# Kernel optimization log

Measured on AMD Instinct MI355X. Metric: run time of the kernel, lower is better.

## Reference

```python
import jax, jax.numpy as jnp
import numpy as np

N = 100000   # nodes
E = 1600000  # edges (avg degree 16)
D = 128      # in_feats
H = 128      # n_hidden
C = 64       # n_classes


def setup_inputs() -> dict:
    key = jax.random.key(0)
    ks = jax.random.split(key, 9)
    x = jax.random.normal(ks[0], (N, D), dtype=jnp.float32)
    src = jax.random.randint(ks[1], (E,), 0, N, dtype=jnp.int32)
    dst = jax.random.randint(ks[2], (E,), 0, N, dtype=jnp.int32)
    s = 1.0 / np.sqrt(D)
    W1 = jax.random.uniform(ks[3], (H, D), jnp.float32, -s, s)
    b1 = jax.random.uniform(ks[4], (H,), jnp.float32, -s, s)
    sh = 1.0 / np.sqrt(H)
    W2 = jax.random.uniform(ks[5], (H, H), jnp.float32, -sh, sh)
    b2 = jax.random.uniform(ks[6], (H,), jnp.float32, -sh, sh)
    W3 = jax.random.uniform(ks[7], (C, H), jnp.float32, -sh, sh)
    b3 = jax.random.uniform(ks[8], (C,), jnp.float32, -sh, sh)
    return {"x": x, "src": src, "dst": dst,
            "W1": W1, "b1": b1, "W2": W2, "b2": b2, "W3": W3, "b3": b3}


def reference(x, src, dst, W1, b1, W2, b2, W3, b3):
    n = x.shape[0]
    # in-degrees of destination nodes (DGL g.in_degrees())
    deg = jax.ops.segment_sum(jnp.ones_like(dst, dtype=x.dtype), dst, num_segments=n)
    norm = 1.0 / (deg + 1.0)  # [N]

    def sage_gcn(h, W, b, act):
        # gather src features, sum into dst (copy_u + sum reduce)
        m = jax.ops.segment_sum(h[src], dst, num_segments=n)  # [N, d]
        h_neigh = (m + h) * norm[:, None]                      # include self, /(deg+1)
        o = h_neigh @ W.T + b                                  # fc_neigh
        return jax.nn.relu(o) if act else o

    h = sage_gcn(x, W1, b1, True)
    h = sage_gcn(h, W2, b2, True)   # dropout is identity in eval mode
    return sage_gcn(h, W3, b3, False)
```

## Files before the change

kernel.cpp:

```cpp
#include <hip/hip_runtime.h>
#include <hip/hip_fp16.h>

typedef _Float16 f16x8 __attribute__((ext_vector_type(8)));
typedef _Float16 f16x4 __attribute__((ext_vector_type(4)));
typedef float    f32x4 __attribute__((ext_vector_type(4)));


#define PSHIFT 6
#define PNODES 64
#define BMAX   2048
#define NBLK   64

__global__ __launch_bounds__(512) void k_hist(const int* __restrict__ dst, int E, int chunk,
                                              int B, int* __restrict__ histT) {
    __shared__ int hist[BMAX];
    int blk = blockIdx.x, t = threadIdx.x;
    for (int k = t; k < B; k += 512) hist[k] = 0;
    __syncthreads();
    int lo = blk * chunk, hi = min(lo + chunk, E);
    for (int i = lo + t; i < hi; i += 512) atomicAdd(&hist[dst[i] >> PSHIFT], 1);
    __syncthreads();
    for (int k = t; k < B; k += 512) histT[k * NBLK + blk] = hist[k];
}

__global__ __launch_bounds__(256) void k_scanA(const int* __restrict__ histT, int total,
                                               int* __restrict__ psum) {
    __shared__ int sd[256];
    int t = threadIdx.x;
    int base = blockIdx.x * 1024 + t * 4;
    int s = 0;
    if (base + 3 < total) {
        int4 v = *(const int4*)(histT + base);
        s = v.x + v.y + v.z + v.w;
    } else {
        for (int j = 0; j < 4; j++) if (base + j < total) s += histT[base + j];
    }
    sd[t] = s;
    __syncthreads();
    for (int off = 128; off > 0; off >>= 1) {
        if (t < off) sd[t] += sd[t + off];
        __syncthreads();
    }
    if (t == 0) psum[blockIdx.x] = sd[0];
}

__global__ __launch_bounds__(128) void k_scanB(const int* __restrict__ psum, int G,
                                               int* __restrict__ pbase,
                                               int* __restrict__ bbase, int B,
                                               int* __restrict__ offsets, int n, int E) {
    __shared__ int sd[128];
    int t = threadIdx.x;
    int v = (t < G) ? psum[t] : 0;
    sd[t] = v;
    __syncthreads();
    int acc = v;
    for (int off = 1; off < 128; off <<= 1) {
        int u = (t >= off) ? sd[t - off] : 0;
        __syncthreads();
        acc += u;
        sd[t] = acc;
        __syncthreads();
    }
    if (t < G) pbase[t] = acc - v;
    if (t == 0) { bbase[B] = E; offsets[n] = E; }
}

__global__ __launch_bounds__(256) void k_scanC(int* __restrict__ histT, int total,
                                               const int* __restrict__ pbase,
                                               int* __restrict__ bbase) {
    __shared__ int sd[256];
    int t = threadIdx.x;
    int base = blockIdx.x * 1024 + t * 4;
    int v[4];
    int s = 0;
    bool full = (base + 3 < total);
    if (full) {
        int4 q = *(const int4*)(histT + base);
        v[0] = q.x; v[1] = q.y; v[2] = q.z; v[3] = q.w;
        s = q.x + q.y + q.z + q.w;
    } else {
#pragma unroll
        for (int j = 0; j < 4; j++) { v[j] = (base + j < total) ? histT[base + j] : 0; s += v[j]; }
    }
    sd[t] = s;
    __syncthreads();
    int acc = s;
    for (int off = 1; off < 256; off <<= 1) {
        int u = (t >= off) ? sd[t - off] : 0;
        __syncthreads();
        acc += u;
        sd[t] = acc;
        __syncthreads();
    }
    int run = pbase[blockIdx.x] + (acc - s);
    int o[4];
#pragma unroll
    for (int j = 0; j < 4; j++) { o[j] = run; run += v[j]; }
    if (full) *(int4*)(histT + base) = make_int4(o[0], o[1], o[2], o[3]);
    else { for (int j = 0; j < 4; j++) if (base + j < total) histT[base + j] = o[j]; }
    if ((base & 63) == 0 && base < total) bbase[base >> 6] = o[0];
}

__global__ __launch_bounds__(512) void k_place(const int* __restrict__ src,
                                               const int* __restrict__ dst,
                                               const int* __restrict__ histT,
                                               int E, int chunk, int B,
                                               unsigned int* __restrict__ ebuf) {
    __shared__ int cur[BMAX];
    int blk = blockIdx.x, t = threadIdx.x;
    for (int k = t; k < B; k += 512) cur[k] = histT[k * NBLK + blk];
    __syncthreads();
    int lo = blk * chunk, hi = min(lo + chunk, E);
    for (int i = lo + t; i < hi; i += 512) {
        int d = dst[i], s = src[i];
        int k = d >> PSHIFT;
        int pos = atomicAdd(&cur[k], 1);
        ebuf[pos] = ((unsigned)(d & (PNODES - 1)) << 17) | (unsigned)s;
    }
}

__global__ __launch_bounds__(256) void k_binB(const unsigned int* __restrict__ ebuf,
                                              const int* __restrict__ bbase,
                                              int* __restrict__ offsets,
                                              float* __restrict__ norm,
                                              int* __restrict__ cols, int n) {
    __shared__ int hist[PNODES];
    __shared__ int lofs[PNODES];
    __shared__ int cur[PNODES];
    int b = blockIdx.x;
    int t = threadIdx.x;
    int base = bbase[b];
    int cnt = bbase[b + 1] - base;
    const unsigned int* bd = ebuf + base;

    if (t < PNODES) hist[t] = 0;
    __syncthreads();
    for (int e = t; e < cnt; e += 256) atomicAdd(&hist[bd[e] >> 17], 1);
    __syncthreads();
    if (t < PNODES) lofs[t] = hist[t];
    __syncthreads();
    for (int off = 1; off < PNODES; off <<= 1) {
        int v = 0;
        if (t < PNODES && t >= off) v = lofs[t - off];
        __syncthreads();
        if (t < PNODES) lofs[t] += v;
        __syncthreads();
    }
    if (t < PNODES) {
        int excl = lofs[t] - hist[t];
        cur[t] = excl;
        int node = (b << PSHIFT) + t;
        if (node < n) {
            offsets[node] = base + excl;
            norm[node] = 1.0f / ((float)hist[t] + 1.0f);
        }
    }
    __syncthreads();
    for (int e = t; e < cnt; e += 256) {
        unsigned v = bd[e];
        int local = v >> 17;
        int s = (int)(v & 0x1FFFF);
        int r = atomicAdd(&cur[local], 1);
        cols[base + r] = s;
    }
}


__global__ __launch_bounds__(256) void k_cvt(const float* __restrict__ x,
                                             _Float16* __restrict__ y, int total8) {
    int i = blockIdx.x * 256 + threadIdx.x;
    if (i >= total8) return;
    float4 a = ((const float4*)x)[i * 2];
    float4 b = ((const float4*)x)[i * 2 + 1];
    f16x8 o;
    o[0] = (_Float16)a.x; o[1] = (_Float16)a.y; o[2] = (_Float16)a.z; o[3] = (_Float16)a.w;
    o[4] = (_Float16)b.x; o[5] = (_Float16)b.y; o[6] = (_Float16)b.z; o[7] = (_Float16)b.w;
    ((f16x8*)y)[i] = o;
}


template <int KOUT, bool IN_F32>
__global__ __launch_bounds__(256) void k_gemm_mfma(const void* __restrict__ Ain,
                                                   const _Float16* __restrict__ Wh,
                                                   _Float16* __restrict__ outh, int n) {
    constexpr int NT = KOUT / 16;
    __shared__ _Float16 A_lds[128 * 136];
    __shared__ _Float16 W_lds[KOUT * 136];

    int tid  = threadIdx.x;
    int lane = tid & 63;
    int wave = tid >> 6;
    int m0   = blockIdx.x * 128;

    for (int i = tid; i < KOUT * 16; i += 256) {
        int r = i >> 4, c = i & 15;
        *(f16x8*)&W_lds[r * 136 + c * 8] = ((const f16x8*)(Wh + r * 128))[c];
    }
    if constexpr (IN_F32) {
        const float* A = (const float*)Ain;
        for (int i = tid; i < 2048; i += 256) {
            int r = i >> 4, c = i & 15;
            int gm = m0 + r;
            f16x8 v = {};
            if (gm < n) {
                float4 u0 = *(const float4*)(A + (size_t)gm * 128 + c * 8);
                float4 u1 = *(const float4*)(A + (size_t)gm * 128 + c * 8 + 4);
                v[0] = (_Float16)u0.x; v[1] = (_Float16)u0.y;
                v[2] = (_Float16)u0.z; v[3] = (_Float16)u0.w;
                v[4] = (_Float16)u1.x; v[5] = (_Float16)u1.y;
                v[6] = (_Float16)u1.z; v[7] = (_Float16)u1.w;
            }
            *(f16x8*)&A_lds[r * 136 + c * 8] = v;
        }
    } else {
        const _Float16* A = (const _Float16*)Ain;
        for (int i = tid; i < 2048; i += 256) {
            int r = i >> 4, c = i & 15;
            int gm = m0 + r;
            f16x8 v = {};
            if (gm < n) v = ((const f16x8*)(A + (size_t)gm * 128))[c];
            *(f16x8*)&A_lds[r * 136 + c * 8] = v;
        }
    }
    __syncthreads();

    int m0w = wave * 32;
    int lr  = lane & 15;
    int lk  = (lane >> 4) * 4;

    f32x4 acc[2][NT];
#pragma unroll
    for (int mi = 0; mi < 2; mi++)
#pragma unroll
        for (int ni = 0; ni < NT; ni++) acc[mi][ni] = (f32x4){0.f, 0.f, 0.f, 0.f};

#pragma unroll
    for (int kk = 0; kk < 8; kk++) {
        int k0 = kk * 16;
        f16x4 a0 = *(const f16x4*)&A_lds[(m0w + lr) * 136 + k0 + lk];
        f16x4 a1 = *(const f16x4*)&A_lds[(m0w + 16 + lr) * 136 + k0 + lk];
#pragma unroll
        for (int ni = 0; ni < NT; ni++) {
            f16x4 b = *(const f16x4*)&W_lds[(ni * 16 + lr) * 136 + k0 + lk];
            acc[0][ni] = __builtin_amdgcn_mfma_f32_16x16x16f16(a0, b, acc[0][ni], 0, 0, 0);
            acc[1][ni] = __builtin_amdgcn_mfma_f32_16x16x16f16(a1, b, acc[1][ni], 0, 0, 0);
        }
    }

    int orow = (lane >> 4) * 4;
#pragma unroll
    for (int mi = 0; mi < 2; mi++) {
#pragma unroll
        for (int r = 0; r < 4; r++) {
            int gm = m0 + m0w + mi * 16 + orow + r;
            if (gm < n) {
                _Float16* op = outh + (size_t)gm * KOUT + lr;
#pragma unroll
                for (int ni = 0; ni < NT; ni++)
                    op[ni * 16] = (_Float16)acc[mi][ni][r];
            }
        }
    }
}


__global__ __launch_bounds__(256) void k_agg128_br(const _Float16* __restrict__ g,
                                                   const int* __restrict__ offs,
                                                   const int* __restrict__ cols,
                                                   const float* __restrict__ norm,
                                                   const float* __restrict__ bias,
                                                   _Float16* __restrict__ hout, int n) {
    int node = blockIdx.x * 16 + (threadIdx.x >> 4);
    if (node >= n) return;
    int lane = threadIdx.x & 15;

    f16x8 sv = ((const f16x8*)(g + (size_t)node * 128))[lane];
    float acc[8];
#pragma unroll
    for (int j = 0; j < 8; j++) acc[j] = (float)sv[j];

    int p = offs[node], e = offs[node + 1];
    for (; p + 4 <= e; p += 4) {
        int c0 = cols[p], c1 = cols[p + 1], c2 = cols[p + 2], c3 = cols[p + 3];
        f16x8 a0 = ((const f16x8*)(g + (size_t)c0 * 128))[lane];
        f16x8 a1 = ((const f16x8*)(g + (size_t)c1 * 128))[lane];
        f16x8 a2 = ((const f16x8*)(g + (size_t)c2 * 128))[lane];
        f16x8 a3 = ((const f16x8*)(g + (size_t)c3 * 128))[lane];
#pragma unroll
        for (int j = 0; j < 8; j++)
            acc[j] += ((float)a0[j] + (float)a1[j]) + ((float)a2[j] + (float)a3[j]);
    }
    for (; p < e; p++) {
        f16x8 a = ((const f16x8*)(g + (size_t)cols[p] * 128))[lane];
#pragma unroll
        for (int j = 0; j < 8; j++) acc[j] += (float)a[j];
    }
    float nm = norm[node];
    float4 bb0 = ((const float4*)bias)[lane * 2];
    float4 bb1 = ((const float4*)bias)[lane * 2 + 1];
    float o[8];
    o[0] = acc[0] * nm + bb0.x; o[1] = acc[1] * nm + bb0.y;
    o[2] = acc[2] * nm + bb0.z; o[3] = acc[3] * nm + bb0.w;
    o[4] = acc[4] * nm + bb1.x; o[5] = acc[5] * nm + bb1.y;
    o[6] = acc[6] * nm + bb1.z; o[7] = acc[7] * nm + bb1.w;
    f16x8 ov;
#pragma unroll
    for (int j = 0; j < 8; j++) ov[j] = (_Float16)fmaxf(o[j], 0.f);
    ((f16x8*)(hout + (size_t)node * 128))[lane] = ov;
}

__global__ __launch_bounds__(256) void k_agg64_b(const _Float16* __restrict__ g,
                                                 const int* __restrict__ offs,
                                                 const int* __restrict__ cols,
                                                 const float* __restrict__ norm,
                                                 const float* __restrict__ bias,
                                                 float* __restrict__ out, int n) {
    int node = blockIdx.x * 32 + (threadIdx.x >> 3);
    if (node >= n) return;
    int lane = threadIdx.x & 7;

    f16x8 sv = ((const f16x8*)(g + (size_t)node * 64))[lane];
    float acc[8];
#pragma unroll
    for (int j = 0; j < 8; j++) acc[j] = (float)sv[j];

    int p = offs[node], e = offs[node + 1];
    for (; p + 4 <= e; p += 4) {
        int c0 = cols[p], c1 = cols[p + 1], c2 = cols[p + 2], c3 = cols[p + 3];
        f16x8 a0 = ((const f16x8*)(g + (size_t)c0 * 64))[lane];
        f16x8 a1 = ((const f16x8*)(g + (size_t)c1 * 64))[lane];
        f16x8 a2 = ((const f16x8*)(g + (size_t)c2 * 64))[lane];
        f16x8 a3 = ((const f16x8*)(g + (size_t)c3 * 64))[lane];
#pragma unroll
        for (int j = 0; j < 8; j++)
            acc[j] += ((float)a0[j] + (float)a1[j]) + ((float)a2[j] + (float)a3[j]);
    }
    for (; p < e; p++) {
        f16x8 a = ((const f16x8*)(g + (size_t)cols[p] * 64))[lane];
#pragma unroll
        for (int j = 0; j < 8; j++) acc[j] += (float)a[j];
    }
    float nm = norm[node];
    float4 bb0 = ((const float4*)bias)[lane * 2];
    float4 bb1 = ((const float4*)bias)[lane * 2 + 1];
    float* op = out + (size_t)node * 64 + lane * 8;
    *(float4*)op = make_float4(acc[0] * nm + bb0.x, acc[1] * nm + bb0.y,
                               acc[2] * nm + bb0.z, acc[3] * nm + bb0.w);
    *(float4*)(op + 4) = make_float4(acc[4] * nm + bb1.x, acc[5] * nm + bb1.y,
                                     acc[6] * nm + bb1.z, acc[7] * nm + bb1.w);
}


extern "C" void kernel_launch(void* const* d_in, const int* in_sizes, int n_in,
                              void* d_out, int out_size, void* d_ws, size_t ws_size,
                              hipStream_t stream) {
    const float* x  = (const float*)d_in[0];
    const int*  src = (const int*)d_in[1];
    const int*  dst = (const int*)d_in[2];
    const float* W1 = (const float*)d_in[3];
    const float* b1 = (const float*)d_in[4];
    const float* W2 = (const float*)d_in[5];
    const float* b2 = (const float*)d_in[6];
    const float* W3 = (const float*)d_in[7];
    const float* b3 = (const float*)d_in[8];
    float* out = (float*)d_out;

    int n = in_sizes[0] / 128;
    int E = in_sizes[1];
    int B = (n + PNODES - 1) >> PSHIFT;
    int total = B * NBLK;
    int chunk = (E + NBLK - 1) / NBLK;
    int G1 = (total + 1023) / 1024;

    char* ws = (char*)d_ws;
    size_t off = 0;
    auto alloc = [&](size_t bytes) -> char* {
        char* p = ws + off;
        off += (bytes + 255) & ~(size_t)255;
        return p;
    };
    int*      bbase   = (int*)alloc(((size_t)B + 1) * 4);
    int*      offsets = (int*)alloc(((size_t)n + 1) * 4);
    float*    norm    = (float*)alloc((size_t)n * 4);
    int*      psum    = (int*)alloc(256 * 4);
    int*      pbase   = (int*)alloc(256 * 4);
    int*      cols    = (int*)alloc((size_t)E * 4);
    _Float16* w1h     = (_Float16*)alloc(128 * 128 * 2);
    _Float16* w2h     = (_Float16*)alloc(128 * 128 * 2);
    _Float16* w3h     = (_Float16*)alloc(64 * 128 * 2);
    _Float16* bufA    = (_Float16*)alloc((size_t)n * 128 * 2);
    _Float16* bufB    = (_Float16*)alloc((size_t)n * 128 * 2);

    unsigned int* ebuf  = (unsigned int*)bufA;
    int*          histT = (int*)((char*)bufA + (size_t)8 * 1024 * 1024);

    k_cvt<<<8, 256, 0, stream>>>(W1, w1h, 2048);
    k_cvt<<<8, 256, 0, stream>>>(W2, w2h, 2048);
    k_cvt<<<4, 256, 0, stream>>>(W3, w3h, 1024);

    k_hist <<<NBLK, 512, 0, stream>>>(dst, E, chunk, B, histT);
    k_scanA<<<G1, 256, 0, stream>>>(histT, total, psum);
    k_scanB<<<1, 128, 0, stream>>>(psum, G1, pbase, bbase, B, offsets, n, E);
    k_scanC<<<G1, 256, 0, stream>>>(histT, total, pbase, bbase);
    k_place<<<NBLK, 512, 0, stream>>>(src, dst, histT, E, chunk, B, ebuf);
    k_binB <<<B, 256, 0, stream>>>(ebuf, bbase, offsets, norm, cols, n);

    int nblkG  = (n + 127) / 128;
    int nblkA  = (n + 15) / 16;
    int nblkA6 = (n + 31) / 32;

    k_gemm_mfma<128, true><<<nblkG, 256, 0, stream>>>(x, w1h, bufA, n);
    k_agg128_br<<<nblkA, 256, 0, stream>>>(bufA, offsets, cols, norm, b1, bufB, n);
    k_gemm_mfma<128, false><<<nblkG, 256, 0, stream>>>(bufB, w2h, bufA, n);
    k_agg128_br<<<nblkA, 256, 0, stream>>>(bufA, offsets, cols, norm, b2, bufB, n);
    k_gemm_mfma<64, false><<<nblkG, 256, 0, stream>>>(bufB, w3h, bufA, n);
    k_agg64_b<<<nblkA6, 256, 0, stream>>>(bufA, offsets, cols, norm, b3, out, n);
}
```

Before: 283.0 us.

## Fuse weight conversion into GEMM, unroll gathers by 8, remap 64-wide aggregation

Removes the three separate weight-conversion kernels by converting fp32 weights to fp16 while loading them into LDS inside each GEMM block. This saves three launches but repeats the conversion in every block. Both aggregation kernels gain an 8-way unrolled neighbour loop so more independent gathers are in flight per thread. The 64-wide aggregation now uses 16 lanes per node with 4-element loads instead of 8 lanes with 8-element loads, giving more threads per node and fewer nodes per block.

```diff
diff --git a/kernel.cpp b/kernel.cpp
--- a/kernel.cpp
+++ b/kernel.cpp
@@ -166,22 +166,9 @@
 }
 
 
-__global__ __launch_bounds__(256) void k_cvt(const float* __restrict__ x,
-                                             _Float16* __restrict__ y, int total8) {
-    int i = blockIdx.x * 256 + threadIdx.x;
-    if (i >= total8) return;
-    float4 a = ((const float4*)x)[i * 2];
-    float4 b = ((const float4*)x)[i * 2 + 1];
-    f16x8 o;
-    o[0] = (_Float16)a.x; o[1] = (_Float16)a.y; o[2] = (_Float16)a.z; o[3] = (_Float16)a.w;
-    o[4] = (_Float16)b.x; o[5] = (_Float16)b.y; o[6] = (_Float16)b.z; o[7] = (_Float16)b.w;
-    ((f16x8*)y)[i] = o;
-}
-
-
 template <int KOUT, bool IN_F32>
 __global__ __launch_bounds__(256) void k_gemm_mfma(const void* __restrict__ Ain,
-                                                   const _Float16* __restrict__ Wh,
+                                                   const float* __restrict__ W,
                                                    _Float16* __restrict__ outh, int n) {
     constexpr int NT = KOUT / 16;
     __shared__ _Float16 A_lds[128 * 136];
@@ -194,7 +181,14 @@
 
     for (int i = tid; i < KOUT * 16; i += 256) {
         int r = i >> 4, c = i & 15;
-        *(f16x8*)&W_lds[r * 136 + c * 8] = ((const f16x8*)(Wh + r * 128))[c];
+        float4 u0 = *(const float4*)(W + (size_t)r * 128 + c * 8);
+        float4 u1 = *(const float4*)(W + (size_t)r * 128 + c * 8 + 4);
+        f16x8 v;
+        v[0] = (_Float16)u0.x; v[1] = (_Float16)u0.y;
+        v[2] = (_Float16)u0.z; v[3] = (_Float16)u0.w;
+        v[4] = (_Float16)u1.x; v[5] = (_Float16)u1.y;
+        v[6] = (_Float16)u1.z; v[7] = (_Float16)u1.w;
+        *(f16x8*)&W_lds[r * 136 + c * 8] = v;
     }
     if constexpr (IN_F32) {
         const float* A = (const float*)Ain;
@@ -280,6 +274,22 @@
     for (int j = 0; j < 8; j++) acc[j] = (float)sv[j];
 
     int p = offs[node], e = offs[node + 1];
+    for (; p + 8 <= e; p += 8) {
+        int c0 = cols[p],     c1 = cols[p + 1], c2 = cols[p + 2], c3 = cols[p + 3];
+        int c4 = cols[p + 4], c5 = cols[p + 5], c6 = cols[p + 6], c7 = cols[p + 7];
+        f16x8 a0 = ((const f16x8*)(g + (size_t)c0 * 128))[lane];
+        f16x8 a1 = ((const f16x8*)(g + (size_t)c1 * 128))[lane];
+        f16x8 a2 = ((const f16x8*)(g + (size_t)c2 * 128))[lane];
+        f16x8 a3 = ((const f16x8*)(g + (size_t)c3 * 128))[lane];
+        f16x8 a4 = ((const f16x8*)(g + (size_t)c4 * 128))[lane];
+        f16x8 a5 = ((const f16x8*)(g + (size_t)c5 * 128))[lane];
+        f16x8 a6 = ((const f16x8*)(g + (size_t)c6 * 128))[lane];
+        f16x8 a7 = ((const f16x8*)(g + (size_t)c7 * 128))[lane];
+#pragma unroll
+        for (int j = 0; j < 8; j++)
+            acc[j] += (((float)a0[j] + (float)a1[j]) + ((float)a2[j] + (float)a3[j]))
+                    + (((float)a4[j] + (float)a5[j]) + ((float)a6[j] + (float)a7[j]));
+    }
     for (; p + 4 <= e; p += 4) {
         int c0 = cols[p], c1 = cols[p + 1], c2 = cols[p + 2], c3 = cols[p + 3];
         f16x8 a0 = ((const f16x8*)(g + (size_t)c0 * 128))[lane];
@@ -315,39 +325,52 @@
                                                  const float* __restrict__ norm,
                                                  const float* __restrict__ bias,
                                                  float* __restrict__ out, int n) {
-    int node = blockIdx.x * 32 + (threadIdx.x >> 3);
+    int node = blockIdx.x * 16 + (threadIdx.x >> 4);
     if (node >= n) return;
-    int lane = threadIdx.x & 7;
-
-    f16x8 sv = ((const f16x8*)(g + (size_t)node * 64))[lane];
-    float acc[8];
-#pragma unroll
-    for (int j = 0; j < 8; j++) acc[j] = (float)sv[j];
+    int lane = threadIdx.x & 15;
+
+    f16x4 sv = ((const f16x4*)(g + (size_t)node * 64))[lane];
+    float acc[4];
+#pragma unroll
+    for (int j = 0; j < 4; j++) acc[j] = (float)sv[j];
 
     int p = offs[node], e = offs[node + 1];
+    for (; p + 8 <= e; p += 8) {
+        int c0 = cols[p],     c1 = cols[p + 1], c2 = cols[p + 2], c3 = cols[p + 3];
+        int c4 = cols[p + 4], c5 = cols[p + 5], c6 = cols[p + 6], c7 = cols[p + 7];
+        f16x4 a0 = ((const f16x4*)(g + (size_t)c0 * 64))[lane];
+        f16x4 a1 = ((const f16x4*)(g + (size_t)c1 * 64))[lane];
+        f16x4 a2 = ((const f16x4*)(g + (size_t)c2 * 64))[lane];
+        f16x4 a3 = ((const f16x4*)(g + (size_t)c3 * 64))[lane];
+        f16x4 a4 = ((const f16x4*)(g + (size_t)c4 * 64))[lane];
+        f16x4 a5 = ((const f16x4*)(g + (size_t)c5 * 64))[lane];
+        f16x4 a6 = ((const f16x4*)(g + (size_t)c6 * 64))[lane];
+        f16x4 a7 = ((const f16x4*)(g + (size_t)c7 * 64))[lane];
+#pragma unroll
+        for (int j = 0; j < 4; j++)
+            acc[j] += (((float)a0[j] + (float)a1[j]) + ((float)a2[j] + (float)a3[j]))
+                    + (((float)a4[j] + (float)a5[j]) + ((float)a6[j] + (float)a7[j]));
+    }
     for (; p + 4 <= e; p += 4) {
         int c0 = cols[p], c1 = cols[p + 1], c2 = cols[p + 2], c3 = cols[p + 3];
-        f16x8 a0 = ((const f16x8*)(g + (size_t)c0 * 64))[lane];
-        f16x8 a1 = ((const f16x8*)(g + (size_t)c1 * 64))[lane];
-        f16x8 a2 = ((const f16x8*)(g + (size_t)c2 * 64))[lane];
-        f16x8 a3 = ((const f16x8*)(g + (size_t)c3 * 64))[lane];
-#pragma unroll
-        for (int j = 0; j < 8; j++)
+        f16x4 a0 = ((const f16x4*)(g + (size_t)c0 * 64))[lane];
+        f16x4 a1 = ((const f16x4*)(g + (size_t)c1 * 64))[lane];
+        f16x4 a2 = ((const f16x4*)(g + (size_t)c2 * 64))[lane];
+        f16x4 a3 = ((const f16x4*)(g + (size_t)c3 * 64))[lane];
+#pragma unroll
+        for (int j = 0; j < 4; j++)
             acc[j] += ((float)a0[j] + (float)a1[j]) + ((float)a2[j] + (float)a3[j]);
     }
     for (; p < e; p++) {
-        f16x8 a = ((const f16x8*)(g + (size_t)cols[p] * 64))[lane];
-#pragma unroll
-        for (int j = 0; j < 8; j++) acc[j] += (float)a[j];
+        f16x4 a = ((const f16x4*)(g + (size_t)cols[p] * 64))[lane];
+#pragma unroll
+        for (int j = 0; j < 4; j++) acc[j] += (float)a[j];
     }
     float nm = norm[node];
-    float4 bb0 = ((const float4*)bias)[lane * 2];
-    float4 bb1 = ((const float4*)bias)[lane * 2 + 1];
-    float* op = out + (size_t)node * 64 + lane * 8;
-    *(float4*)op = make_float4(acc[0] * nm + bb0.x, acc[1] * nm + bb0.y,
-                               acc[2] * nm + bb0.z, acc[3] * nm + bb0.w);
-    *(float4*)(op + 4) = make_float4(acc[4] * nm + bb1.x, acc[5] * nm + bb1.y,
-                                     acc[6] * nm + bb1.z, acc[7] * nm + bb1.w);
+    float4 bb = ((const float4*)bias)[lane];
+    float* op = out + (size_t)node * 64 + lane * 4;
+    *(float4*)op = make_float4(acc[0] * nm + bb.x, acc[1] * nm + bb.y,
+                               acc[2] * nm + bb.z, acc[3] * nm + bb.w);
 }
 
 
@@ -385,18 +408,11 @@
     int*      psum    = (int*)alloc(256 * 4);
     int*      pbase   = (int*)alloc(256 * 4);
     int*      cols    = (int*)alloc((size_t)E * 4);
-    _Float16* w1h     = (_Float16*)alloc(128 * 128 * 2);
-    _Float16* w2h     = (_Float16*)alloc(128 * 128 * 2);
-    _Float16* w3h     = (_Float16*)alloc(64 * 128 * 2);
     _Float16* bufA    = (_Float16*)alloc((size_t)n * 128 * 2);
     _Float16* bufB    = (_Float16*)alloc((size_t)n * 128 * 2);
 
     unsigned int* ebuf  = (unsigned int*)bufA;
     int*          histT = (int*)((char*)bufA + (size_t)8 * 1024 * 1024);
-
-    k_cvt<<<8, 256, 0, stream>>>(W1, w1h, 2048);
-    k_cvt<<<8, 256, 0, stream>>>(W2, w2h, 2048);
-    k_cvt<<<4, 256, 0, stream>>>(W3, w3h, 1024);
 
     k_hist <<<NBLK, 512, 0, stream>>>(dst, E, chunk, B, histT);
     k_scanA<<<G1, 256, 0, stream>>>(histT, total, psum);
@@ -405,14 +421,13 @@
     k_place<<<NBLK, 512, 0, stream>>>(src, dst, histT, E, chunk, B, ebuf);
     k_binB <<<B, 256, 0, stream>>>(ebuf, bbase, offsets, norm, cols, n);
 
-    int nblkG  = (n + 127) / 128;
-    int nblkA  = (n + 15) / 16;
-    int nblkA6 = (n + 31) / 32;
-
-    k_gemm_mfma<128, true><<<nblkG, 256, 0, stream>>>(x, w1h, bufA, n);
+    int nblkG = (n + 127) / 128;
+    int nblkA = (n + 15) / 16;
+
+    k_gemm_mfma<128, true><<<nblkG, 256, 0, stream>>>(x, W1, bufA, n);
     k_agg128_br<<<nblkA, 256, 0, stream>>>(bufA, offsets, cols, norm, b1, bufB, n);
-    k_gemm_mfma<128, false><<<nblkG, 256, 0, stream>>>(bufB, w2h, bufA, n);
+    k_gemm_mfma<128, false><<<nblkG, 256, 0, stream>>>(bufB, W2, bufA, n);
     k_agg128_br<<<nblkA, 256, 0, stream>>>(bufA, offsets, cols, norm, b2, bufB, n);
-    k_gemm_mfma<64, false><<<nblkG, 256, 0, stream>>>(bufB, w3h, bufA, n);
-    k_agg64_b<<<nblkA6, 256, 0, stream>>>(bufA, offsets, cols, norm, b3, out, n);
-}
+    k_gemm_mfma<64, false><<<nblkG, 256, 0, stream>>>(bufB, W3, bufA, n);
+    k_agg64_b<<<nblkA, 256, 0, stream>>>(bufA, offsets, cols, norm, b3, out, n);
+}
```

New measurement: 280.3 us. Within noise of the previous version (-1.0%).

## Slice aggregation by feature columns, split GEMM output, merge weight conversions, widen histogram

Applied to the files above, without the earlier changes.

The aggregation kernels now assign each block a 16-column feature slice for 128 nodes. Each node is handled by two threads reading 16 bytes each, where previously 16 or 8 threads shared one node's full row. Column indices are read with nontemporal loads. The idea is to keep each slice's gather working set small enough to stay in cache, at the cost of re-reading the CSR indices once per slice. The GEMM now processes output columns in 64-wide halves to reduce weight LDS. The three weight conversions are merged into one launch, and the histogram/placement grid doubles to 128 blocks, with the scan adjusted to match.

```diff
diff --git a/kernel.cpp b/kernel.cpp
--- a/kernel.cpp
+++ b/kernel.cpp
@@ -9,7 +9,7 @@
 #define PSHIFT 6
 #define PNODES 64
 #define BMAX   2048
-#define NBLK   64
+#define NBLK   128
 
 __global__ __launch_bounds__(512) void k_hist(const int* __restrict__ dst, int E, int chunk,
                                               int B, int* __restrict__ histT) {
@@ -44,17 +44,17 @@
     if (t == 0) psum[blockIdx.x] = sd[0];
 }
 
-__global__ __launch_bounds__(128) void k_scanB(const int* __restrict__ psum, int G,
+__global__ __launch_bounds__(256) void k_scanB(const int* __restrict__ psum, int G,
                                                int* __restrict__ pbase,
                                                int* __restrict__ bbase, int B,
                                                int* __restrict__ offsets, int n, int E) {
-    __shared__ int sd[128];
+    __shared__ int sd[256];
     int t = threadIdx.x;
     int v = (t < G) ? psum[t] : 0;
     sd[t] = v;
     __syncthreads();
     int acc = v;
-    for (int off = 1; off < 128; off <<= 1) {
+    for (int off = 1; off < 256; off <<= 1) {
         int u = (t >= off) ? sd[t - off] : 0;
         __syncthreads();
         acc += u;
@@ -98,7 +98,7 @@
     for (int j = 0; j < 4; j++) { o[j] = run; run += v[j]; }
     if (full) *(int4*)(histT + base) = make_int4(o[0], o[1], o[2], o[3]);
     else { for (int j = 0; j < 4; j++) if (base + j < total) histT[base + j] = o[j]; }
-    if ((base & 63) == 0 && base < total) bbase[base >> 6] = o[0];
+    if ((base & (NBLK - 1)) == 0 && base < total) bbase[base / NBLK] = o[0];
 }
 
 __global__ __launch_bounds__(512) void k_place(const int* __restrict__ src,
@@ -166,35 +166,41 @@
 }
 
 
-__global__ __launch_bounds__(256) void k_cvt(const float* __restrict__ x,
-                                             _Float16* __restrict__ y, int total8) {
+__global__ __launch_bounds__(256) void k_cvtW(const float* __restrict__ W1,
+                                              const float* __restrict__ W2,
+                                              const float* __restrict__ W3,
+                                              _Float16* __restrict__ w16) {
     int i = blockIdx.x * 256 + threadIdx.x;
-    if (i >= total8) return;
-    float4 a = ((const float4*)x)[i * 2];
-    float4 b = ((const float4*)x)[i * 2 + 1];
-    f16x8 o;
-    o[0] = (_Float16)a.x; o[1] = (_Float16)a.y; o[2] = (_Float16)a.z; o[3] = (_Float16)a.w;
-    o[4] = (_Float16)b.x; o[5] = (_Float16)b.y; o[6] = (_Float16)b.z; o[7] = (_Float16)b.w;
-    ((f16x8*)y)[i] = o;
+    if (i >= 5120) return;
+    int idx = i * 8;
+    const float* src;
+    if (idx < 16384)      src = W1 + idx;
+    else if (idx < 32768) src = W2 + (idx - 16384);
+    else                  src = W3 + (idx - 32768);
+    float4 a = *(const float4*)src;
+    float4 b = *(const float4*)(src + 4);
+    f16x8 v;
+    v[0] = (_Float16)a.x; v[1] = (_Float16)a.y; v[2] = (_Float16)a.z; v[3] = (_Float16)a.w;
+    v[4] = (_Float16)b.x; v[5] = (_Float16)b.y; v[6] = (_Float16)b.z; v[7] = (_Float16)b.w;
+    *(f16x8*)(w16 + idx) = v;
 }
 
 
 template <int KOUT, bool IN_F32>
 __global__ __launch_bounds__(256) void k_gemm_mfma(const void* __restrict__ Ain,
-                                                   const _Float16* __restrict__ Wh,
+                                                   const _Float16* __restrict__ W16,
                                                    _Float16* __restrict__ outh, int n) {
-    constexpr int NT = KOUT / 16;
     __shared__ _Float16 A_lds[128 * 136];
-    __shared__ _Float16 W_lds[KOUT * 136];
+    __shared__ _Float16 W_lds[64 * 136];
 
     int tid  = threadIdx.x;
     int lane = tid & 63;
     int wave = tid >> 6;
     int m0   = blockIdx.x * 128;
 
-    for (int i = tid; i < KOUT * 16; i += 256) {
+    for (int i = tid; i < 64 * 16; i += 256) {
         int r = i >> 4, c = i & 15;
-        *(f16x8*)&W_lds[r * 136 + c * 8] = ((const f16x8*)(Wh + r * 128))[c];
+        *(f16x8*)&W_lds[r * 136 + c * 8] = *(const f16x8*)(W16 + (size_t)r * 128 + c * 8);
     }
     if constexpr (IN_F32) {
         const float* A = (const float*)Ain;
@@ -227,77 +233,97 @@
     int m0w = wave * 32;
     int lr  = lane & 15;
     int lk  = (lane >> 4) * 4;
-
-    f32x4 acc[2][NT];
-#pragma unroll
-    for (int mi = 0; mi < 2; mi++)
-#pragma unroll
-        for (int ni = 0; ni < NT; ni++) acc[mi][ni] = (f32x4){0.f, 0.f, 0.f, 0.f};
-
-#pragma unroll
-    for (int kk = 0; kk < 8; kk++) {
-        int k0 = kk * 16;
-        f16x4 a0 = *(const f16x4*)&A_lds[(m0w + lr) * 136 + k0 + lk];
-        f16x4 a1 = *(const f16x4*)&A_lds[(m0w + 16 + lr) * 136 + k0 + lk];
-#pragma unroll
-        for (int ni = 0; ni < NT; ni++) {
-            f16x4 b = *(const f16x4*)&W_lds[(ni * 16 + lr) * 136 + k0 + lk];
-            acc[0][ni] = __builtin_amdgcn_mfma_f32_16x16x16f16(a0, b, acc[0][ni], 0, 0, 0);
-            acc[1][ni] = __builtin_amdgcn_mfma_f32_16x16x16f16(a1, b, acc[1][ni], 0, 0, 0);
-        }
-    }
-
     int orow = (lane >> 4) * 4;
-#pragma unroll
-    for (int mi = 0; mi < 2; mi++) {
-#pragma unroll
-        for (int r = 0; r < 4; r++) {
-            int gm = m0 + m0w + mi * 16 + orow + r;
-            if (gm < n) {
-                _Float16* op = outh + (size_t)gm * KOUT + lr;
-#pragma unroll
-                for (int ni = 0; ni < NT; ni++)
-                    op[ni * 16] = (_Float16)acc[mi][ni][r];
+
+#pragma unroll
+    for (int hf = 0; hf < KOUT / 64; hf++) {
+        if (hf > 0) {
+            __syncthreads();
+            for (int i = tid; i < 64 * 16; i += 256) {
+                int r = i >> 4, c = i & 15;
+                *(f16x8*)&W_lds[r * 136 + c * 8] =
+                    *(const f16x8*)(W16 + (size_t)(hf * 64 + r) * 128 + c * 8);
             }
-        }
-    }
-}
-
-
-__global__ __launch_bounds__(256) void k_agg128_br(const _Float16* __restrict__ g,
-                                                   const int* __restrict__ offs,
-                                                   const int* __restrict__ cols,
-                                                   const float* __restrict__ norm,
-                                                   const float* __restrict__ bias,
-                                                   _Float16* __restrict__ hout, int n) {
-    int node = blockIdx.x * 16 + (threadIdx.x >> 4);
+            __syncthreads();
+        }
+
+        f32x4 acc[2][4];
+#pragma unroll
+        for (int mi = 0; mi < 2; mi++)
+#pragma unroll
+            for (int ni = 0; ni < 4; ni++) acc[mi][ni] = (f32x4){0.f, 0.f, 0.f, 0.f};
+
+#pragma unroll
+        for (int kk = 0; kk < 8; kk++) {
+            int k0 = kk * 16;
+            f16x4 a0 = *(const f16x4*)&A_lds[(m0w + lr) * 136 + k0 + lk];
+            f16x4 a1 = *(const f16x4*)&A_lds[(m0w + 16 + lr) * 136 + k0 + lk];
+#pragma unroll
+            for (int ni = 0; ni < 4; ni++) {
+                f16x4 b = *(const f16x4*)&W_lds[(ni * 16 + lr) * 136 + k0 + lk];
+                acc[0][ni] = __builtin_amdgcn_mfma_f32_16x16x16f16(a0, b, acc[0][ni], 0, 0, 0);
+                acc[1][ni] = __builtin_amdgcn_mfma_f32_16x16x16f16(a1, b, acc[1][ni], 0, 0, 0);
+            }
+        }
+
+#pragma unroll
+        for (int mi = 0; mi < 2; mi++) {
+#pragma unroll
+            for (int r = 0; r < 4; r++) {
+                int gm = m0 + m0w + mi * 16 + orow + r;
+                if (gm < n) {
+                    _Float16* op = outh + (size_t)gm * KOUT + hf * 64 + lr;
+#pragma unroll
+                    for (int ni = 0; ni < 4; ni++)
+                        op[ni * 16] = (_Float16)acc[mi][ni][r];
+                }
+            }
+        }
+    }
+}
+
+
+__global__ __launch_bounds__(256) void k_agg128_slice(const _Float16* __restrict__ g,
+                                                      const int* __restrict__ offs,
+                                                      const int* __restrict__ cols,
+                                                      const float* __restrict__ norm,
+                                                      const float* __restrict__ bias,
+                                                      _Float16* __restrict__ hout, int n) {
+    int s     = blockIdx.x & 7;
+    int chunk = blockIdx.x >> 3;
+    int node  = chunk * 128 + (threadIdx.x >> 1);
     if (node >= n) return;
-    int lane = threadIdx.x & 15;
-
-    f16x8 sv = ((const f16x8*)(g + (size_t)node * 128))[lane];
+    int l2 = threadIdx.x & 1;
+    const _Float16* gs = g + s * 16 + l2 * 8;
+
+    f16x8 sv = *(const f16x8*)(gs + (size_t)node * 128);
     float acc[8];
 #pragma unroll
     for (int j = 0; j < 8; j++) acc[j] = (float)sv[j];
 
     int p = offs[node], e = offs[node + 1];
     for (; p + 4 <= e; p += 4) {
-        int c0 = cols[p], c1 = cols[p + 1], c2 = cols[p + 2], c3 = cols[p + 3];
-        f16x8 a0 = ((const f16x8*)(g + (size_t)c0 * 128))[lane];
-        f16x8 a1 = ((const f16x8*)(g + (size_t)c1 * 128))[lane];
-        f16x8 a2 = ((const f16x8*)(g + (size_t)c2 * 128))[lane];
-        f16x8 a3 = ((const f16x8*)(g + (size_t)c3 * 128))[lane];
+        int c0 = __builtin_nontemporal_load(cols + p);
+        int c1 = __builtin_nontemporal_load(cols + p + 1);
+        int c2 = __builtin_nontemporal_load(cols + p + 2);
+        int c3 = __builtin_nontemporal_load(cols + p + 3);
+        f16x8 a0 = *(const f16x8*)(gs + (size_t)c0 * 128);
+        f16x8 a1 = *(const f16x8*)(gs + (size_t)c1 * 128);
+        f16x8 a2 = *(const f16x8*)(gs + (size_t)c2 * 128);
+        f16x8 a3 = *(const f16x8*)(gs + (size_t)c3 * 128);
 #pragma unroll
         for (int j = 0; j < 8; j++)
             acc[j] += ((float)a0[j] + (float)a1[j]) + ((float)a2[j] + (float)a3[j]);
     }
     for (; p < e; p++) {
-        f16x8 a = ((const f16x8*)(g + (size_t)cols[p] * 128))[lane];
+        int c = __builtin_nontemporal_load(cols + p);
+        f16x8 a = *(const f16x8*)(gs + (size_t)c * 128);
 #pragma unroll
         for (int j = 0; j < 8; j++) acc[j] += (float)a[j];
     }
     float nm = norm[node];
-    float4 bb0 = ((const float4*)bias)[lane * 2];
-    float4 bb1 = ((const float4*)bias)[lane * 2 + 1];
+    float4 bb0 = *(const float4*)(bias + s * 16 + l2 * 8);
+    float4 bb1 = *(const float4*)(bias + s * 16 + l2 * 8 + 4);
     float o[8];
     o[0] = acc[0] * nm + bb0.x; o[1] = acc[1] * nm + bb0.y;
     o[2] = acc[2] * nm + bb0.z; o[3] = acc[3] * nm + bb0.w;
@@ -306,44 +332,51 @@
     f16x8 ov;
 #pragma unroll
     for (int j = 0; j < 8; j++) ov[j] = (_Float16)fmaxf(o[j], 0.f);
-    ((f16x8*)(hout + (size_t)node * 128))[lane] = ov;
-}
-
-__global__ __launch_bounds__(256) void k_agg64_b(const _Float16* __restrict__ g,
-                                                 const int* __restrict__ offs,
-                                                 const int* __restrict__ cols,
-                                                 const float* __restrict__ norm,
-                                                 const float* __restrict__ bias,
-                                                 float* __restrict__ out, int n) {
-    int node = blockIdx.x * 32 + (threadIdx.x >> 3);
+    *(f16x8*)(hout + (size_t)node * 128 + s * 16 + l2 * 8) = ov;
+}
+
+__global__ __launch_bounds__(256) void k_agg64_slice(const _Float16* __restrict__ g,
+                                                     const int* __restrict__ offs,
+                                                     const int* __restrict__ cols,
+                                                     const float* __restrict__ norm,
+                                                     const float* __restrict__ bias,
+                                                     float* __restrict__ out, int n) {
+    int s     = blockIdx.x & 3;
+    int chunk = blockIdx.x >> 2;
+    int node  = chunk * 128 + (threadIdx.x >> 1);
     if (node >= n) return;
-    int lane = threadIdx.x & 7;
-
-    f16x8 sv = ((const f16x8*)(g + (size_t)node * 64))[lane];
+    int l2 = threadIdx.x & 1;
+    const _Float16* gs = g + s * 16 + l2 * 8;
+
+    f16x8 sv = *(const f16x8*)(gs + (size_t)node * 64);
     float acc[8];
 #pragma unroll
     for (int j = 0; j < 8; j++) acc[j] = (float)sv[j];
 
     int p = offs[node], e = offs[node + 1];
     for (; p + 4 <= e; p += 4) {
-        int c0 = cols[p], c1 = cols[p + 1], c2 = cols[p + 2], c3 = cols[p + 3];
-        f16x8 a0 = ((const f16x8*)(g + (size_t)c0 * 64))[lane];
-        f16x8 a1 = ((const f16x8*)(g + (size_t)c1 * 64))[lane];
-        f16x8 a2 = ((const f16x8*)(g + (size_t)c2 * 64))[lane];
-        f16x8 a3 = ((const f16x8*)(g + (size_t)c3 * 64))[lane];
+        int c0 = __builtin_nontemporal_load(cols + p);
+        int c1 = __builtin_nontemporal_load(cols + p + 1);
+        int c2 = __builtin_nontemporal_load(cols + p + 2);
+        int c3 = __builtin_nontemporal_load(cols + p + 3);
+        f16x8 a0 = *(const f16x8*)(gs + (size_t)c0 * 64);
+        f16x8 a1 = *(const f16x8*)(gs + (size_t)c1 * 64);
+        f16x8 a2 = *(const f16x8*)(gs + (size_t)c2 * 64);
+        f16x8 a3 = *(const f16x8*)(gs + (size_t)c3 * 64);
 #pragma unroll
         for (int j = 0; j < 8; j++)
             acc[j] += ((float)a0[j] + (float)a1[j]) + ((float)a2[j] + (float)a3[j]);
     }
     for (; p < e; p++) {
-        f16x8 a = ((const f16x8*)(g + (size_t)cols[p] * 64))[lane];
+        int c = __builtin_nontemporal_load(cols + p);
+        f16x8 a = *(const f16x8*)(gs + (size_t)c * 64);
 #pragma unroll
         for (int j = 0; j < 8; j++) acc[j] += (float)a[j];
     }
     float nm = norm[node];
-    float4 bb0 = ((const float4*)bias)[lane * 2];
-    float4 bb1 = ((const float4*)bias)[lane * 2 + 1];
-    float* op = out + (size_t)node * 64 + lane * 8;
+    float4 bb0 = *(const float4*)(bias + s * 16 + l2 * 8);
+    float4 bb1 = *(const float4*)(bias + s * 16 + l2 * 8 + 4);
+    float* op = out + (size_t)node * 64 + s * 16 + l2 * 8;
     *(float4*)op = make_float4(acc[0] * nm + bb0.x, acc[1] * nm + bb0.y,
                                acc[2] * nm + bb0.z, acc[3] * nm + bb0.w);
     *(float4*)(op + 4) = make_float4(acc[4] * nm + bb1.x, acc[5] * nm + bb1.y,
@@ -385,34 +418,29 @@
     int*      psum    = (int*)alloc(256 * 4);
     int*      pbase   = (int*)alloc(256 * 4);
     int*      cols    = (int*)alloc((size_t)E * 4);
-    _Float16* w1h     = (_Float16*)alloc(128 * 128 * 2);
-    _Float16* w2h     = (_Float16*)alloc(128 * 128 * 2);
-    _Float16* w3h     = (_Float16*)alloc(64 * 128 * 2);
+    _Float16* w16     = (_Float16*)alloc(40960 * 2);
     _Float16* bufA    = (_Float16*)alloc((size_t)n * 128 * 2);
     _Float16* bufB    = (_Float16*)alloc((size_t)n * 128 * 2);
 
     unsigned int* ebuf  = (unsigned int*)bufA;
     int*          histT = (int*)((char*)bufA + (size_t)8 * 1024 * 1024);
 
-    k_cvt<<<8, 256, 0, stream>>>(W1, w1h, 2048);
-    k_cvt<<<8, 256, 0, stream>>>(W2, w2h, 2048);
-    k_cvt<<<4, 256, 0, stream>>>(W3, w3h, 1024);
+    k_cvtW<<<20, 256, 0, stream>>>(W1, W2, W3, w16);
 
     k_hist <<<NBLK, 512, 0, stream>>>(dst, E, chunk, B, histT);
     k_scanA<<<G1, 256, 0, stream>>>(histT, total, psum);
-    k_scanB<<<1, 128, 0, stream>>>(psum, G1, pbase, bbase, B, offsets, n, E);
+    k_scanB<<<1, 256, 0, stream>>>(psum, G1, pbase, bbase, B, offsets, n, E);
     k_scanC<<<G1, 256, 0, stream>>>(histT, total, pbase, bbase);
     k_place<<<NBLK, 512, 0, stream>>>(src, dst, histT, E, chunk, B, ebuf);
     k_binB <<<B, 256, 0, stream>>>(ebuf, bbase, offsets, norm, cols, n);
 
-    int nblkG  = (n + 127) / 128;
-    int nblkA  = (n + 15) / 16;
-    int nblkA6 = (n + 31) / 32;
-
-    k_gemm_mfma<128, true><<<nblkG, 256, 0, stream>>>(x, w1h, bufA, n);
-    k_agg128_br<<<nblkA, 256, 0, stream>>>(bufA, offsets, cols, norm, b1, bufB, n);
-    k_gemm_mfma<128, false><<<nblkG, 256, 0, stream>>>(bufB, w2h, bufA, n);
-    k_agg128_br<<<nblkA, 256, 0, stream>>>(bufA, offsets, cols, norm, b2, bufB, n);
-    k_gemm_mfma<64, false><<<nblkG, 256, 0, stream>>>(bufB, w3h, bufA, n);
-    k_agg64_b<<<nblkA6, 256, 0, stream>>>(bufA, offsets, cols, norm, b3, out, n);
-}
+    int nblkG = (n + 127) / 128;
+    int nchunk = (n + 127) / 128;
+
+    k_gemm_mfma<128, true><<<nblkG, 256, 0, stream>>>(x, w16, bufA, n);
+    k_agg128_slice<<<nchunk * 8, 256, 0, stream>>>(bufA, offsets, cols, norm, b1, bufB, n);
+    k_gemm_mfma<128, false><<<nblkG, 256, 0, stream>>>(bufB, w16 + 16384, bufA, n);
+    k_agg128_slice<<<nchunk * 8, 256, 0, stream>>>(bufA, offsets, cols, norm, b2, bufB, n);
+    k_gemm_mfma<64, false><<<nblkG, 256, 0, stream>>>(bufB, w16 + 32768, bufA, n);
+    k_agg64_slice<<<nchunk * 4, 256, 0, stream>>>(bufA, offsets, cols, norm, b3, out, n);
+}
```

Result: slower. 682.0 us (+141.0%).
